# Kernel optimization log

Hardware: AMD Instinct MI355X
Metric: run time of the kernel (lower is better)

## Reference

```python
import jax, jax.numpy as jnp
import numpy as np
from jax import lax

KS = 3
PAD = 1
N = KS * KS


def setup_inputs() -> dict:
    key = jax.random.key(0)
    k1, k2, k3, k4, k5, k6 = jax.random.split(key, 6)
    b, cin, cout, h, w = 4, 64, 64, 256, 256
    x = jax.random.normal(k1, (b, cin, h, w), jnp.float32)
    # offset-predicting conv: 2*N output channels, 3x3, pad 1
    p_conv_w = 0.1 * jax.random.normal(k2, (2 * N, cin, KS, KS), jnp.float32)
    p_conv_b = jnp.zeros((2 * N,), jnp.float32)
    # main conv applied to the k*k-expanded sampled map (no bias in original)
    conv_w = jax.random.normal(k3, (cout, cin, KS, KS), jnp.float32) / np.sqrt(cin * N)
    bn_gamma = 1.0 + 0.1 * jax.random.normal(k4, (cout,), jnp.float32)
    bn_beta = 0.1 * jax.random.normal(k5, (cout,), jnp.float32)
    return {"x": x, "p_conv_w": p_conv_w, "p_conv_b": p_conv_b,
            "conv_w": conv_w, "bn_gamma": bn_gamma, "bn_beta": bn_beta}


def _deform_conv(x, p_conv_w, p_conv_b, conv_w, bn_gamma, bn_beta):
    b, c, h, w = x.shape
    # offsets: (b, 2N, h, w) -> (b, h, w, 2N)
    offset = lax.conv_general_dilated(x, p_conv_w, (1, 1), ((PAD, PAD), (PAD, PAD)))
    offset = offset + p_conv_b[None, :, None, None]
    offset = jnp.transpose(offset, (0, 2, 3, 1))
    # zero-pad input; sampling coordinates live on the padded grid
    x_pad = jnp.pad(x, ((0, 0), (0, 0), (PAD, PAD), (PAD, PAD)))
    Hp, Wp = h + 2 * PAD, w + 2 * PAD
    # p = p_0 + p_n + offset  (x/y coords each of shape (b,h,w,N))
    r = jnp.arange(-(KS - 1) // 2, KS // 2 + 1, dtype=jnp.float32)  # [-1,0,1]
    pn_x, pn_y = jnp.meshgrid(r, r, indexing="ij")
    pn_x, pn_y = pn_x.reshape(-1), pn_y.reshape(-1)  # (N,)
    p0_x = jnp.arange(1, h + 1, dtype=jnp.float32)[:, None, None]  # (h,1,1)
    p0_y = jnp.arange(1, w + 1, dtype=jnp.float32)[None, :, None]  # (1,w,1)
    p_x = offset[..., :N] + p0_x + pn_x  # (b,h,w,N)
    p_y = offset[..., N:] + p0_y + pn_y
    # integer corner coords (detached / non-differentiable), clamped
    fx = jnp.floor(lax.stop_gradient(p_x))
    fy = jnp.floor(lax.stop_gradient(p_y))
    q_lt_x = jnp.clip(fx, 0, Hp - 1).astype(jnp.int32)
    q_lt_y = jnp.clip(fy, 0, Wp - 1).astype(jnp.int32)
    q_rb_x = jnp.clip(fx + 1, 0, Hp - 1).astype(jnp.int32)
    q_rb_y = jnp.clip(fy + 1, 0, Wp - 1).astype(jnp.int32)
    # clamped continuous coords (gradient flows to offsets)
    px = jnp.clip(p_x, 0, Hp - 1)
    py = jnp.clip(p_y, 0, Wp - 1)
    # bilinear weights
    ltx = q_lt_x.astype(px.dtype); lty = q_lt_y.astype(px.dtype)
    rbx = q_rb_x.astype(px.dtype); rby = q_rb_y.astype(px.dtype)
    g_lt = (1 + (ltx - px)) * (1 + (lty - py))
    g_rb = (1 - (rbx - px)) * (1 - (rby - py))
    g_lb = (1 + (ltx - px)) * (1 - (rby - py))
    g_rt = (1 - (rbx - px)) * (1 + (lty - py))
    x_flat = x_pad.reshape(b, c, Hp * Wp)

    def gather(qx, qy):
        idx = (qx * Wp + qy).reshape(b, 1, -1)  # (b,1,h*w*N)
        out = jnp.take_along_axis(x_flat, idx, axis=2)
        return out.reshape(b, c, h, w, N)

    x_off = (g_lt[:, None] * gather(q_lt_x, q_lt_y)
             + g_rb[:, None] * gather(q_rb_x, q_rb_y)
             + g_lb[:, None] * gather(q_lt_x, q_rb_y)
             + g_rt[:, None] * gather(q_rb_x, q_lt_y))  # (b,c,h,w,N)
    # conv (kernel=KS, stride=KS on k*k-expanded map) == contraction over (c,N)
    out = jnp.einsum("bchwn,ocn->bohw", x_off, conv_w.reshape(conv_w.shape[0], c, N))
    # BatchNorm2d (training-mode batch statistics) + LeakyReLU(0.1)
    mean = out.mean(axis=(0, 2, 3), keepdims=True)
    var = out.var(axis=(0, 2, 3), keepdims=True)
    y = (out - mean) * lax.rsqrt(var + 1e-5)
    y = y * bn_gamma[None, :, None, None] + bn_beta[None, :, None, None]
    return jnp.where(y > 0, y, 0.1 * y)


def reference(x, p_conv_w, p_conv_b, conv_w, bn_gamma, bn_beta):
    return _deform_conv(x, p_conv_w, p_conv_b, conv_w, bn_gamma, bn_beta)
```

## Files before the change

### kernel.cpp

```cpp
#include <hip/hip_runtime.h>
#include <math.h>

#define BB 4
#define CC 64
#define OCC 64
#define HH 256
#define WW 256
#define HP 258
#define WP 258
#define NPIX (BB * HH * WW)
#define CNT_F 262144.0f

typedef __attribute__((ext_vector_type(8))) __bf16 bf16x8;
typedef __attribute__((ext_vector_type(4))) float f32x4;

__device__ __forceinline__ float blo(unsigned u) {
    return __builtin_bit_cast(float, u << 16);
}
__device__ __forceinline__ float bhi(unsigned u) {
    return __builtin_bit_cast(float, u & 0xffff0000u);
}

__global__ __launch_bounds__(256) void prep(const float* __restrict__ x,
                                            __bf16* __restrict__ xt,
                                            const float* __restrict__ cw,
                                            const float* __restrict__ pw,
                                            __bf16* __restrict__ wtb,
                                            __bf16* __restrict__ pwb,
                                            float* __restrict__ stats) {
    int blk = blockIdx.x;
    int tid = threadIdx.x;
    if (blk < 4096) {
        int xchunk = blk & 3;
        int y = (blk >> 2) & 255;
        int b = blk >> 10;
        __shared__ float tile[64][65];
        int x0 = xchunk * 64;
        int col = tid & 63;
        int crow = tid >> 6;
        const float* xp = x + ((size_t)b * CC) * HH * WW + (size_t)y * WW + x0;
#pragma unroll
        for (int i = 0; i < 16; ++i) {
            int c = crow + i * 4;
            tile[c][col] = xp[(size_t)c * HH * WW + col];
        }
        __syncthreads();
        __bf16* op = xt + (((size_t)b * HP + (y + 1)) * WP + (x0 + 1)) * CC;
        int c0 = (tid & 15) * 4;
        int xg = tid >> 4;
#pragma unroll
        for (int i = 0; i < 4; ++i) {
            int xl = xg + i * 16;
            __bf16 v0 = (__bf16)tile[c0 + 0][xl];
            __bf16 v1 = (__bf16)tile[c0 + 1][xl];
            __bf16 v2 = (__bf16)tile[c0 + 2][xl];
            __bf16 v3 = (__bf16)tile[c0 + 3][xl];
            ushort4 rv;
            rv.x = __builtin_bit_cast(unsigned short, v0);
            rv.y = __builtin_bit_cast(unsigned short, v1);
            rv.z = __builtin_bit_cast(unsigned short, v2);
            rv.w = __builtin_bit_cast(unsigned short, v3);
            *(ushort4*)&op[(size_t)xl * CC + c0] = rv;
        }
    } else if (blk < 5124) {
        int i = (blk - 4096) * 256 + tid;
        const int total = BB * 1028 * CC;
        if (i >= total) return;
        int c = i & 63;
        int p = (i >> 6) % 1028;
        int b = (i >> 6) / 1028;
        int yp, xp;
        if (p < 258)      { yp = 0;           xp = p; }
        else if (p < 516) { yp = 257;         xp = p - 258; }
        else if (p < 772) { yp = p - 516 + 1; xp = 0; }
        else              { yp = p - 772 + 1; xp = 257; }
        xt[(((size_t)b * HP + yp) * WP + xp) * CC + c] = (__bf16)0.0f;
    } else if (blk < 5340) {
        int i = (blk - 5124) * 256 + tid;
        if (i < 36864) {
            int c = i & 63;
            int n = (i >> 6) % 9;
            int oc = i / 576;
            wtb[i] = (__bf16)cw[((size_t)oc * CC + c) * 9 + n];
        } else {
            int j = i - 36864;
            if (j >= 18432) return;
            int c = j & 63;
            int n = (j >> 6) % 9;
            int oc = j / 576;
            pwb[j] = (__bf16)(oc < 18 ? pw[((size_t)oc * CC + c) * 9 + n] : 0.0f);
        }
    } else {
        if (tid < 128) stats[tid] = 0.0f;
    }
}

__global__ __launch_bounds__(512, 6) void deform_fused(const __bf16* __restrict__ xt,
                                                       const __bf16* __restrict__ pwb,
                                                       const float* __restrict__ pb,
                                                       const __bf16* __restrict__ wtb,
                                                       float* __restrict__ out,
                                                       float* __restrict__ partials) {
    int phys = blockIdx.x;
    int blk = (phys & 7) * 1024 + (phys >> 3);
    int xq = blk & 7;
    int y  = (blk >> 3) & 255;
    int b  = blk >> 11;
    int x0 = xq * 32;
    int tid = threadIdx.x;
    int wave = tid >> 6, lane = tid & 63;
    int chp = lane & 31, half = lane >> 5;

    __shared__ __attribute__((aligned(16))) char smem[41472];
    __bf16 (*sS)[34][72] = (__bf16 (*)[34][72])smem;
    char* sAb = smem;
    float* offp = (float*)(smem + 36864);

    {
        const char* base = (const char*)xt + (size_t)b * HP * WP * CC * 2;
        for (int t = tid; t < 816; t += 512) {
            int pos = t >> 3, c8 = t & 7;
            int r = pos / 34, j = pos - r * 34;
            uint4 d = *(const uint4*)(base
                + (size_t)((y + r) * WP + (x0 + j)) * (CC * 2) + c8 * 16);
            *(uint4*)&sS[r][j][c8 * 8] = d;
        }
    }
    __syncthreads();

    {
        int mh = wave & 1;
        int nh = (wave >> 1) & 1;
        int kh = wave >> 2;
        int m = lane & 15, q = lane >> 4;
        int p_a = mh * 16 + m;
        f32x4 acc = {0.0f, 0.0f, 0.0f, 0.0f};
        const __bf16* bp = pwb + (size_t)(nh * 16 + m) * 576 + q * 8;
        if (kh == 0) {
#pragma unroll
            for (int n = 0; n < 5; ++n) {
                int dy = n / 3, dx = n - dy * 3;
                const __bf16* abase = &sS[dy][p_a + dx][q * 8];
#pragma unroll
                for (int h = 0; h < 2; ++h) {
                    bf16x8 a  = *(const bf16x8*)(abase + h * 32);
                    bf16x8 bv = *(const bf16x8*)(bp + n * 64 + h * 32);
                    acc = __builtin_amdgcn_mfma_f32_16x16x32_bf16(a, bv, acc, 0, 0, 0);
                }
            }
        } else {
#pragma unroll
            for (int n = 5; n < 9; ++n) {
                int dy = n / 3, dx = n - dy * 3;
                const __bf16* abase = &sS[dy][p_a + dx][q * 8];
#pragma unroll
                for (int h = 0; h < 2; ++h) {
                    bf16x8 a  = *(const bf16x8*)(abase + h * 32);
                    bf16x8 bv = *(const bf16x8*)(bp + n * 64 + h * 32);
                    acc = __builtin_amdgcn_mfma_f32_16x16x32_bf16(a, bv, acc, 0, 0, 0);
                }
            }
        }
        int oc = nh * 16 + m;
        if (oc < 18) {
            float bias = (kh == 0) ? pb[oc] : 0.0f;
            float* obf = offp + kh * 576;
#pragma unroll
            for (int r = 0; r < 4; ++r)
                obf[(mh * 16 + q * 4 + r) * 18 + oc] = acc[r] + bias;
        }
    }
    __syncthreads();

    float g0 = 0.0f, g1 = 0.0f, g2 = 0.0f, g3 = 0.0f;
    int c0 = 0, c1 = 0, c2 = 0, c3 = 0;
    if (lane < 36) {
        int t = wave * 36 + lane;
        int n = t >> 5, p = t & 31;
        float offx = offp[p * 18 + n]     + offp[576 + p * 18 + n];
        float offy = offp[p * 18 + n + 9] + offp[576 + p * 18 + n + 9];
        float px = offx + (float)(y + 1) + (float)(n / 3 - 1);
        float py = offy + (float)(x0 + p + 1) + (float)(n % 3 - 1);
        float fx = floorf(px), fy = floorf(py);
        float pxc = fminf(fmaxf(px, 0.0f), 257.0f);
        float pyc = fminf(fmaxf(py, 0.0f), 257.0f);
        int ltx = (int)fminf(fmaxf(fx, 0.0f), 257.0f);
        int lty = (int)fminf(fmaxf(fy, 0.0f), 257.0f);
        int rbx = (int)fminf(fmaxf(fx + 1.0f, 0.0f), 257.0f);
        int rby = (int)fminf(fmaxf(fy + 1.0f, 0.0f), 257.0f);
        float dxl = 1.0f + ((float)ltx - pxc);
        float dxr = 1.0f - ((float)rbx - pxc);
        float dyl = 1.0f + ((float)lty - pyc);
        float dyr = 1.0f - ((float)rby - pyc);
        g0 = dxl * dyl;
        g1 = dxr * dyr;
        g2 = dxl * dyr;
        g3 = dxr * dyl;
        c0 = ((ltx * WP + lty) * CC) * 2;
        c1 = ((rbx * WP + rby) * CC) * 2;
        c2 = ((ltx * WP + rby) * CC) * 2;
        c3 = ((rbx * WP + lty) * CC) * 2;
    }

    {
        const char* xbl = (const char*)xt + (size_t)b * HP * WP * CC * 2 + (size_t)chp * 4;
#pragma unroll 3
        for (int r = 0; r < 18; ++r) {
            int src = r * 2 + half;
            float gx = __shfl(g0, src, 64);
            float gy = __shfl(g1, src, 64);
            float gz = __shfl(g2, src, 64);
            float gw = __shfl(g3, src, 64);
            int vx = __shfl(c0, src, 64);
            int vy = __shfl(c1, src, 64);
            int vz = __shfl(c2, src, 64);
            int vw = __shfl(c3, src, 64);
            unsigned d0 = *(const unsigned*)(xbl + vx);
            unsigned d1 = *(const unsigned*)(xbl + vy);
            unsigned d2 = *(const unsigned*)(xbl + vz);
            unsigned d3 = *(const unsigned*)(xbl + vw);
            float lo = gx * blo(d0) + gy * blo(d1) + gz * blo(d2) + gw * blo(d3);
            float hi = gx * bhi(d0) + gy * bhi(d1) + gz * bhi(d2) + gw * bhi(d3);
            __bf16 rlo = (__bf16)lo, rhi = (__bf16)hi;
            ushort2 rv;
            rv.x = __builtin_bit_cast(unsigned short, rlo);
            rv.y = __builtin_bit_cast(unsigned short, rhi);
            int t = wave * 36 + src;
            int n = t >> 5, p = t & 31;
            unsigned bo = (unsigned)p * 1152u + (unsigned)n * 128u + (unsigned)chp * 4u;
            bo ^= (unsigned)((p & 7) << 4);
            *(ushort2*)(sAb + bo) = rv;
        }
    }
    __syncthreads();

    int m = lane & 15, q = lane >> 4;
    int ph = wave >> 2;
    int oc = (wave & 3) * 16 + m;
    f32x4 acc = {0.0f, 0.0f, 0.0f, 0.0f};
    {
        int prow = ph * 16 + m;
        unsigned rowb = (unsigned)prow * 1152u;
        unsigned key = (unsigned)((prow & 7) << 4);
        const __bf16* bp = wtb + (size_t)oc * 576 + q * 8;
        __builtin_amdgcn_s_setprio(1);
#pragma unroll
        for (int k0 = 0; k0 < 576; k0 += 32) {
            unsigned bo = rowb + (((unsigned)(k0 * 2 + q * 16)) ^ key);
            bf16x8 a  = *(const bf16x8*)(sAb + bo);
            bf16x8 bv = *(const bf16x8*)(bp + k0);
            acc = __builtin_amdgcn_mfma_f32_16x16x32_bf16(a, bv, acc, 0, 0, 0);
        }
        __builtin_amdgcn_s_setprio(0);
    }

    float* ob = out + (((size_t)b * OCC + oc) * HH + y) * WW + x0 + ph * 16 + q * 4;
    float4 v;
    v.x = acc[0]; v.y = acc[1]; v.z = acc[2]; v.w = acc[3];
    *(float4*)ob = v;

    {
        float s  = acc[0] + acc[1] + acc[2] + acc[3];
        float sq = acc[0] * acc[0] + acc[1] * acc[1]
                 + acc[2] * acc[2] + acc[3] * acc[3];
        s  += __shfl_xor(s, 16, 64);
        sq += __shfl_xor(sq, 16, 64);
        s  += __shfl_xor(s, 32, 64);
        sq += __shfl_xor(sq, 32, 64);
        if (q == 0) {
            float* pp = partials + ((size_t)phys * 2 + ph) * 128;
            pp[oc] = s;
            pp[64 + oc] = sq;
        }
    }
}

__global__ __launch_bounds__(256) void stats_reduce(const float* __restrict__ partials,
                                                    float* __restrict__ stats) {
    __shared__ float sacc[8][128];
    int tid = threadIdx.x;
    int cg = tid & 31;
    int rg = tid >> 5;
    float a0 = 0.0f, a1 = 0.0f, a2 = 0.0f, a3 = 0.0f;
    const float* base = partials + ((size_t)blockIdx.x * 256 + rg) * 128 + cg * 4;
#pragma unroll 4
    for (int r = 0; r < 32; ++r) {
        float4 v = *(const float4*)(base + (size_t)r * 8 * 128);
        a0 += v.x; a1 += v.y; a2 += v.z; a3 += v.w;
    }
    sacc[rg][cg * 4 + 0] = a0;
    sacc[rg][cg * 4 + 1] = a1;
    sacc[rg][cg * 4 + 2] = a2;
    sacc[rg][cg * 4 + 3] = a3;
    __syncthreads();
    if (tid < 128) {
        float s = 0.0f;
#pragma unroll
        for (int g = 0; g < 8; ++g) s += sacc[g][tid];
        atomicAdd(&stats[tid], s);
    }
}

__global__ __launch_bounds__(256) void bn_leaky(float* __restrict__ out,
                                                const float* __restrict__ stats,
                                                const float* __restrict__ gamma,
                                                const float* __restrict__ beta) {
    int i = blockIdx.x * 256 + threadIdx.x;
    int oc = (i >> 14) & 63;
    float mean = stats[oc] * (1.0f / CNT_F);
    float var = stats[64 + oc] * (1.0f / CNT_F) - mean * mean;
    float scale = gamma[oc] * rsqrtf(var + 1e-5f);
    float shift = beta[oc] - mean * scale;
    float4* o4 = (float4*)out;
    float4 v = o4[i];
    v.x = v.x * scale + shift; v.x = v.x > 0.0f ? v.x : 0.1f * v.x;
    v.y = v.y * scale + shift; v.y = v.y > 0.0f ? v.y : 0.1f * v.y;
    v.z = v.z * scale + shift; v.z = v.z > 0.0f ? v.z : 0.1f * v.z;
    v.w = v.w * scale + shift; v.w = v.w > 0.0f ? v.w : 0.1f * v.w;
    o4[i] = v;
}

extern "C" void kernel_launch(void* const* d_in, const int* in_sizes, int n_in,
                              void* d_out, int out_size, void* d_ws, size_t ws_size,
                              hipStream_t stream) {
    (void)in_sizes; (void)n_in; (void)out_size; (void)ws_size;
    const float* x     = (const float*)d_in[0];
    const float* pw    = (const float*)d_in[1];
    const float* pb    = (const float*)d_in[2];
    const float* cw    = (const float*)d_in[3];
    const float* gamma = (const float*)d_in[4];
    const float* beta  = (const float*)d_in[5];
    float* out = (float*)d_out;
    char* ws = (char*)d_ws;

    __bf16* xtb  = (__bf16*)ws;
    float* partials = (float*)(ws + 34080768);
    __bf16* wtb  = (__bf16*)(ws + 34080768 + 18874368);
    __bf16* pwb  = (__bf16*)(ws + 34080768 + 18874368 + 73728);
    float*  stats = (float*)(ws + 34080768 + 18874368 + 73728 + 36864);

    prep<<<5341, 256, 0, stream>>>(x, xtb, cw, pw, wtb, pwb, stats);
    deform_fused<<<8192, 512, 0, stream>>>(xtb, pwb, pb, wtb, out, partials);
    stats_reduce<<<64, 256, 0, stream>>>(partials, stats);
    bn_leaky<<<NPIX * OCC / 4 / 256, 256, 0, stream>>>(out, stats, gamma, beta);
}
```

Baseline: 374.4 us.

## Fuse all stages into one persistent cooperative kernel with grid syncs

New measurement: 971.4 us. +159.5%, slower.

```diff
diff --git a/kernel.cpp b/kernel.cpp
--- a/kernel.cpp
+++ b/kernel.cpp
@@ -1,5 +1,8 @@
 #include <hip/hip_runtime.h>
+#include <hip/hip_cooperative_groups.h>
 #include <math.h>
+
+namespace cg = cooperative_groups;
 
 #define BB 4
 #define CC 64
@@ -10,6 +13,9 @@
 #define WP 258
 #define NPIX (BB * HH * WW)
 #define CNT_F 262144.0f
+#define NBLK 768
+#define NTHR 512
+#define GSZ (NBLK * NTHR)
 
 typedef __attribute__((ext_vector_type(8))) __bf16 bf16x8;
 typedef __attribute__((ext_vector_type(4))) float f32x4;
@@ -20,6 +26,7 @@
 __device__ __forceinline__ float bhi(unsigned u) {
     return __builtin_bit_cast(float, u & 0xffff0000u);
 }
+
 
 __global__ __launch_bounds__(256) void prep(const float* __restrict__ x,
                                             __bf16* __restrict__ xt,
@@ -320,6 +327,313 @@
     o4[i] = v;
 }
 
+__global__ __launch_bounds__(NTHR, 6) void mega(const float* __restrict__ x,
+                                                const float* __restrict__ pw,
+                                                const float* __restrict__ pb,
+                                                const float* __restrict__ cw,
+                                                const float* __restrict__ gamma,
+                                                const float* __restrict__ beta,
+                                                __bf16* __restrict__ xt,
+                                                __bf16* __restrict__ wtb,
+                                                __bf16* __restrict__ pwb,
+                                                float* __restrict__ out,
+                                                float* __restrict__ partials,
+                                                float* __restrict__ stats) {
+    cg::grid_group grid = cg::this_grid();
+    int tid = threadIdx.x;
+    int gid = blockIdx.x * NTHR + tid;
+
+    __shared__ __attribute__((aligned(16))) char smem[41472];
+
+    {
+        float (*tile)[65] = (float (*)[65])smem;
+        for (int v = blockIdx.x; v < 4096; v += NBLK) {
+            int xchunk = v & 3;
+            int y = (v >> 2) & 255;
+            int b = v >> 10;
+            int x0 = xchunk * 64;
+            int col = tid & 63;
+            int crow = tid >> 6;
+            const float* xp = x + ((size_t)b * CC) * HH * WW + (size_t)y * WW + x0;
+#pragma unroll
+            for (int i = 0; i < 8; ++i) {
+                int c = crow + i * 8;
+                tile[c][col] = xp[(size_t)c * HH * WW + col];
+            }
+            __syncthreads();
+            __bf16* op = xt + (((size_t)b * HP + (y + 1)) * WP + (x0 + 1)) * CC;
+            int c0 = (tid & 15) * 4;
+            int xg = tid >> 4;
+#pragma unroll
+            for (int i = 0; i < 2; ++i) {
+                int xl = xg + i * 32;
+                __bf16 v0 = (__bf16)tile[c0 + 0][xl];
+                __bf16 v1 = (__bf16)tile[c0 + 1][xl];
+                __bf16 v2 = (__bf16)tile[c0 + 2][xl];
+                __bf16 v3 = (__bf16)tile[c0 + 3][xl];
+                ushort4 rv;
+                rv.x = __builtin_bit_cast(unsigned short, v0);
+                rv.y = __builtin_bit_cast(unsigned short, v1);
+                rv.z = __builtin_bit_cast(unsigned short, v2);
+                rv.w = __builtin_bit_cast(unsigned short, v3);
+                *(ushort4*)&op[(size_t)xl * CC + c0] = rv;
+            }
+            __syncthreads();
+        }
+    }
+    for (int i = gid; i < BB * 1028 * CC; i += GSZ) {
+        int c = i & 63;
+        int p = (i >> 6) % 1028;
+        int b = (i >> 6) / 1028;
+        int yp, xp;
+        if (p < 258)      { yp = 0;           xp = p; }
+        else if (p < 516) { yp = 257;         xp = p - 258; }
+        else if (p < 772) { yp = p - 516 + 1; xp = 0; }
+        else              { yp = p - 772 + 1; xp = 257; }
+        xt[(((size_t)b * HP + yp) * WP + xp) * CC + c] = (__bf16)0.0f;
+    }
+    for (int i = gid; i < 55296; i += GSZ) {
+        if (i < 36864) {
+            int c = i & 63;
+            int n = (i >> 6) % 9;
+            int oc = i / 576;
+            wtb[i] = (__bf16)cw[((size_t)oc * CC + c) * 9 + n];
+        } else {
+            int j = i - 36864;
+            int c = j & 63;
+            int n = (j >> 6) % 9;
+            int oc = j / 576;
+            pwb[j] = (__bf16)(oc < 18 ? pw[((size_t)oc * CC + c) * 9 + n] : 0.0f);
+        }
+    }
+    if (gid < 128) stats[gid] = 0.0f;
+
+    __threadfence();
+    grid.sync();
+
+    {
+        __bf16 (*sS)[34][72] = (__bf16 (*)[34][72])smem;
+        char* sAb = smem;
+        float* offp = (float*)(smem + 36864);
+        int wave = tid >> 6, lane = tid & 63;
+        int chp = lane & 31, half = lane >> 5;
+
+        for (int v = blockIdx.x; v < 8192; v += NBLK) {
+            int blk = (v & 7) * 1024 + (v >> 3);
+            int xq = blk & 7;
+            int y  = (blk >> 3) & 255;
+            int b  = blk >> 11;
+            int x0 = xq * 32;
+
+            {
+                const char* base = (const char*)xt + (size_t)b * HP * WP * CC * 2;
+                for (int t = tid; t < 816; t += NTHR) {
+                    int pos = t >> 3, c8 = t & 7;
+                    int r = pos / 34, j = pos - r * 34;
+                    uint4 d = *(const uint4*)(base
+                        + (size_t)((y + r) * WP + (x0 + j)) * (CC * 2) + c8 * 16);
+                    *(uint4*)&sS[r][j][c8 * 8] = d;
+                }
+            }
+            __syncthreads();
+
+            {
+                int mh = wave & 1;
+                int nh = (wave >> 1) & 1;
+                int kh = wave >> 2;
+                int m = lane & 15, q = lane >> 4;
+                int p_a = mh * 16 + m;
+                f32x4 acc = {0.0f, 0.0f, 0.0f, 0.0f};
+                const __bf16* bp = pwb + (size_t)(nh * 16 + m) * 576 + q * 8;
+                if (kh == 0) {
+#pragma unroll
+                    for (int n = 0; n < 5; ++n) {
+                        int dy = n / 3, dx = n - dy * 3;
+                        const __bf16* abase = &sS[dy][p_a + dx][q * 8];
+#pragma unroll
+                        for (int h = 0; h < 2; ++h) {
+                            bf16x8 a  = *(const bf16x8*)(abase + h * 32);
+                            bf16x8 bv = *(const bf16x8*)(bp + n * 64 + h * 32);
+                            acc = __builtin_amdgcn_mfma_f32_16x16x32_bf16(a, bv, acc, 0, 0, 0);
+                        }
+                    }
+                } else {
+#pragma unroll
+                    for (int n = 5; n < 9; ++n) {
+                        int dy = n / 3, dx = n - dy * 3;
+                        const __bf16* abase = &sS[dy][p_a + dx][q * 8];
+#pragma unroll
+                        for (int h = 0; h < 2; ++h) {
+                            bf16x8 a  = *(const bf16x8*)(abase + h * 32);
+                            bf16x8 bv = *(const bf16x8*)(bp + n * 64 + h * 32);
+                            acc = __builtin_amdgcn_mfma_f32_16x16x32_bf16(a, bv, acc, 0, 0, 0);
+                        }
+                    }
+                }
+                int oc = nh * 16 + m;
+                if (oc < 18) {
+                    float bias = (kh == 0) ? pb[oc] : 0.0f;
+                    float* obf = offp + kh * 576;
+#pragma unroll
+                    for (int r = 0; r < 4; ++r)
+                        obf[(mh * 16 + q * 4 + r) * 18 + oc] = acc[r] + bias;
+                }
+            }
+            __syncthreads();
+
+            float g0 = 0.0f, g1 = 0.0f, g2 = 0.0f, g3 = 0.0f;
+            int c0 = 0, c1 = 0, c2 = 0, c3 = 0;
+            if (lane < 36) {
+                int t = wave * 36 + lane;
+                int n = t >> 5, p = t & 31;
+                float offx = offp[p * 18 + n]     + offp[576 + p * 18 + n];
+                float offy = offp[p * 18 + n + 9] + offp[576 + p * 18 + n + 9];
+                float px = offx + (float)(y + 1) + (float)(n / 3 - 1);
+                float py = offy + (float)(x0 + p + 1) + (float)(n % 3 - 1);
+                float fx = floorf(px), fy = floorf(py);
+                float pxc = fminf(fmaxf(px, 0.0f), 257.0f);
+                float pyc = fminf(fmaxf(py, 0.0f), 257.0f);
+                int ltx = (int)fminf(fmaxf(fx, 0.0f), 257.0f);
+                int lty = (int)fminf(fmaxf(fy, 0.0f), 257.0f);
+                int rbx = (int)fminf(fmaxf(fx + 1.0f, 0.0f), 257.0f);
+                int rby = (int)fminf(fmaxf(fy + 1.0f, 0.0f), 257.0f);
+                float dxl = 1.0f + ((float)ltx - pxc);
+                float dxr = 1.0f - ((float)rbx - pxc);
+                float dyl = 1.0f + ((float)lty - pyc);
+                float dyr = 1.0f - ((float)rby - pyc);
+                g0 = dxl * dyl;
+                g1 = dxr * dyr;
+                g2 = dxl * dyr;
+                g3 = dxr * dyl;
+                c0 = ((ltx * WP + lty) * CC) * 2;
+                c1 = ((rbx * WP + rby) * CC) * 2;
+                c2 = ((ltx * WP + rby) * CC) * 2;
+                c3 = ((rbx * WP + lty) * CC) * 2;
+            }
+
+            {
+                const char* xbl = (const char*)xt + (size_t)b * HP * WP * CC * 2 + (size_t)chp * 4;
+#pragma unroll 3
+                for (int r = 0; r < 18; ++r) {
+                    int src = r * 2 + half;
+                    float gx = __shfl(g0, src, 64);
+                    float gy = __shfl(g1, src, 64);
+                    float gz = __shfl(g2, src, 64);
+                    float gw = __shfl(g3, src, 64);
+                    int vx = __shfl(c0, src, 64);
+                    int vy = __shfl(c1, src, 64);
+                    int vz = __shfl(c2, src, 64);
+                    int vw = __shfl(c3, src, 64);
+                    unsigned d0 = *(const unsigned*)(xbl + vx);
+                    unsigned d1 = *(const unsigned*)(xbl + vy);
+                    unsigned d2 = *(const unsigned*)(xbl + vz);
+                    unsigned d3 = *(const unsigned*)(xbl + vw);
+                    float lo = gx * blo(d0) + gy * blo(d1) + gz * blo(d2) + gw * blo(d3);
+                    float hi = gx * bhi(d0) + gy * bhi(d1) + gz * bhi(d2) + gw * bhi(d3);
+                    __bf16 rlo = (__bf16)lo, rhi = (__bf16)hi;
+                    ushort2 rv;
+                    rv.x = __builtin_bit_cast(unsigned short, rlo);
+                    rv.y = __builtin_bit_cast(unsigned short, rhi);
+                    int t = wave * 36 + src;
+                    int n = t >> 5, p = t & 31;
+                    unsigned bo = (unsigned)p * 1152u + (unsigned)n * 128u + (unsigned)chp * 4u;
+                    bo ^= (unsigned)((p & 7) << 4);
+                    *(ushort2*)(sAb + bo) = rv;
+                }
+            }
+            __syncthreads();
+
+            int m = lane & 15, q = lane >> 4;
+            int ph = wave >> 2;
+            int oc = (wave & 3) * 16 + m;
+            f32x4 acc = {0.0f, 0.0f, 0.0f, 0.0f};
+            {
+                int prow = ph * 16 + m;
+                unsigned rowb = (unsigned)prow * 1152u;
+                unsigned key = (unsigned)((prow & 7) << 4);
+                const __bf16* bp = wtb + (size_t)oc * 576 + q * 8;
+                __builtin_amdgcn_s_setprio(1);
+#pragma unroll
+                for (int k0 = 0; k0 < 576; k0 += 32) {
+                    unsigned bo = rowb + (((unsigned)(k0 * 2 + q * 16)) ^ key);
+                    bf16x8 a  = *(const bf16x8*)(sAb + bo);
+                    bf16x8 bv = *(const bf16x8*)(bp + k0);
+                    acc = __builtin_amdgcn_mfma_f32_16x16x32_bf16(a, bv, acc, 0, 0, 0);
+                }
+                __builtin_amdgcn_s_setprio(0);
+            }
+
+            float* ob = out + (((size_t)b * OCC + oc) * HH + y) * WW + x0 + ph * 16 + q * 4;
+            float4 vv;
+            vv.x = acc[0]; vv.y = acc[1]; vv.z = acc[2]; vv.w = acc[3];
+            *(float4*)ob = vv;
+
+            {
+                float s  = acc[0] + acc[1] + acc[2] + acc[3];
+                float sq = acc[0] * acc[0] + acc[1] * acc[1]
+                         + acc[2] * acc[2] + acc[3] * acc[3];
+                s  += __shfl_xor(s, 16, 64);
+                sq += __shfl_xor(sq, 16, 64);
+                s  += __shfl_xor(s, 32, 64);
+                sq += __shfl_xor(sq, 32, 64);
+                if (q == 0) {
+                    float* pp = partials + ((size_t)v * 2 + ph) * 128;
+                    pp[oc] = s;
+                    pp[64 + oc] = sq;
+                }
+            }
+            __syncthreads();
+        }
+    }
+
+    __threadfence();
+    grid.sync();
+
+    if (blockIdx.x < 64) {
+        float (*sacc)[128] = (float (*)[128])smem;
+        int cgq = tid & 31;
+        int rg = tid >> 5;
+        float a0 = 0.0f, a1 = 0.0f, a2 = 0.0f, a3 = 0.0f;
+        const float* base = partials + ((size_t)blockIdx.x * 256 + rg) * 128 + cgq * 4;
+#pragma unroll 4
+        for (int r = 0; r < 16; ++r) {
+            float4 v = *(const float4*)(base + (size_t)r * 16 * 128);
+            a0 += v.x; a1 += v.y; a2 += v.z; a3 += v.w;
+        }
+        sacc[rg][cgq * 4 + 0] = a0;
+        sacc[rg][cgq * 4 + 1] = a1;
+        sacc[rg][cgq * 4 + 2] = a2;
+        sacc[rg][cgq * 4 + 3] = a3;
+        __syncthreads();
+        if (tid < 128) {
+            float s = 0.0f;
+#pragma unroll
+            for (int g = 0; g < 16; ++g) s += sacc[g][tid];
+            atomicAdd(&stats[tid], s);
+        }
+    }
+
+    __threadfence();
+    grid.sync();
+
+    {
+        float4* o4 = (float4*)out;
+        for (int i = gid; i < NPIX * OCC / 4; i += GSZ) {
+            int oc = (i >> 14) & 63;
+            float mean = stats[oc] * (1.0f / CNT_F);
+            float var = stats[64 + oc] * (1.0f / CNT_F) - mean * mean;
+            float scale = gamma[oc] * rsqrtf(var + 1e-5f);
+            float shift = beta[oc] - mean * scale;
+            float4 v = o4[i];
+            v.x = v.x * scale + shift; v.x = v.x > 0.0f ? v.x : 0.1f * v.x;
+            v.y = v.y * scale + shift; v.y = v.y > 0.0f ? v.y : 0.1f * v.y;
+            v.z = v.z * scale + shift; v.z = v.z > 0.0f ? v.z : 0.1f * v.z;
+            v.w = v.w * scale + shift; v.w = v.w > 0.0f ? v.w : 0.1f * v.w;
+            o4[i] = v;
+        }
+    }
+}
+
 extern "C" void kernel_launch(void* const* d_in, const int* in_sizes, int n_in,
                               void* d_out, int out_size, void* d_ws, size_t ws_size,
                               hipStream_t stream) {
@@ -339,8 +653,17 @@
     __bf16* pwb  = (__bf16*)(ws + 34080768 + 18874368 + 73728);
     float*  stats = (float*)(ws + 34080768 + 18874368 + 73728 + 36864);
 
-    prep<<<5341, 256, 0, stream>>>(x, xtb, cw, pw, wtb, pwb, stats);
-    deform_fused<<<8192, 512, 0, stream>>>(xtb, pwb, pb, wtb, out, partials);
-    stats_reduce<<<64, 256, 0, stream>>>(partials, stats);
-    bn_leaky<<<NPIX * OCC / 4 / 256, 256, 0, stream>>>(out, stats, gamma, beta);
-}
+    void* kargs[] = {
+        (void*)&x, (void*)&pw, (void*)&pb, (void*)&cw, (void*)&gamma, (void*)&beta,
+        (void*)&xtb, (void*)&wtb, (void*)&pwb, (void*)&out, (void*)&partials, (void*)&stats
+    };
+    hipError_t err = hipLaunchCooperativeKernel(
+        reinterpret_cast<const void*>(&mega), dim3(NBLK), dim3(NTHR), kargs, 0, stream);
+    if (err != hipSuccess) {
+        (void)hipGetLastError();
+        prep<<<5341, 256, 0, stream>>>(x, xtb, cw, pw, wtb, pwb, stats);
+        deform_fused<<<8192, 512, 0, stream>>>(xtb, pwb, pb, wtb, out, partials);
+        stats_reduce<<<64, 256, 0, stream>>>(partials, stats);
+        bn_leaky<<<NPIX * OCC / 4 / 256, 256, 0, stream>>>(out, stats, gamma, beta);
+    }
+}
```
